# Kernel optimization log

Measured on AMD Instinct MI355X. Metric: run time of the kernel, lower is better.

Reference implementation:

```python
import jax, jax.numpy as jnp
import numpy as np

IN_F = 1024
OUT_F = 1024
N_ORDER = 13  # grid_size=10 + spline_order=3
RMS_EPS = 1e-6


def setup_inputs() -> dict:
    key = jax.random.key(0)
    k_x, k_b, k_p = jax.random.split(key, 3)
    x = jax.random.normal(k_x, (4, 2048, IN_F), dtype=jnp.float32)
    # flax param init: normal(stddev=scale_base/sqrt(in_features)) etc.
    base_weight = jax.random.normal(k_b, (IN_F, OUT_F), dtype=jnp.float32) * (1.0 / np.sqrt(IN_F))
    poly_weight = jax.random.normal(k_p, (N_ORDER, IN_F, OUT_F), dtype=jnp.float32) * (0.1 / np.sqrt(IN_F * N_ORDER))
    rms_scale = jnp.ones((OUT_F,), dtype=jnp.float32)  # nn.RMSNorm default scale init
    return {"x": x, "base_weight": base_weight, "poly_weight": poly_weight, "rms_scale": rms_scale}


def reference(x, base_weight, poly_weight, rms_scale):
    orig_dtype = x.dtype
    prefix = x.shape[:-1]
    x_2d = x.reshape(-1, IN_F)  # [B, in]

    # Base path: SiLU(x) @ W_base in bf16
    x_c = x_2d.astype(jnp.bfloat16)
    out = jax.nn.silu(x_c) @ base_weight.astype(jnp.bfloat16)  # [B, out] bf16

    # Chebyshev recursion on tanh-normalized fp32 input
    x_safe = jnp.tanh(x_2d.astype(jnp.float32))
    pw = poly_weight.astype(jnp.bfloat16)
    T_prev = jnp.ones_like(x_safe)
    T_curr = x_safe
    out = out + T_prev.astype(jnp.bfloat16) @ pw[0]
    out = out + T_curr.astype(jnp.bfloat16) @ pw[1]
    for k in range(2, N_ORDER):  # fixed small unroll (13 orders)
        T_next = 2.0 * x_safe * T_curr - T_prev
        out = out + T_next.astype(jnp.bfloat16) @ pw[k]
        T_prev = T_curr
        T_curr = T_next

    # RMSNorm (flax default: eps=1e-6, learned scale)
    o32 = out.astype(jnp.float32)
    ms = jnp.mean(o32 * o32, axis=-1, keepdims=True)
    o32 = o32 * jax.lax.rsqrt(ms + RMS_EPS) * rms_scale
    return o32.astype(orig_dtype).reshape(prefix + (OUT_F,))
```

## Files before the change

kernel.cpp:

```cpp
#include <hip/hip_runtime.h>
#include <cstdint>

#define IN_F  1024
#define OUT_F 1024
#define NORD  13
#define BROWS 8192

typedef __bf16 bf16x8 __attribute__((ext_vector_type(8)));
typedef float  f32x4  __attribute__((ext_vector_type(4)));
typedef unsigned short u16x8 __attribute__((ext_vector_type(8)));
typedef unsigned short u16x4 __attribute__((ext_vector_type(4)));

__device__ __forceinline__ unsigned short f2bf(float f) {
  unsigned int u = __float_as_uint(f);
  unsigned int r = u + 0x7FFFu + ((u >> 16) & 1u);
  return (unsigned short)(r >> 16);
}
__device__ __forceinline__ float bf2f(unsigned short h) {
  return __uint_as_float(((unsigned int)h) << 16);
}
__device__ __forceinline__ float bfround(float f) { return bf2f(f2bf(f)); }

__device__ __forceinline__ float fast_tanh(float x) {
  float e = __expf(2.0f * x);
  return 1.0f - 2.0f / (e + 1.0f);
}

__device__ __forceinline__ void gload_lds16(const void* g, void* l) {
  __builtin_amdgcn_global_load_lds(
      (__attribute__((address_space(1))) unsigned int*)(uintptr_t)g,
      (__attribute__((address_space(3))) unsigned int*)(unsigned int)(uintptr_t)l,
      16, 0, 0);
}

__global__ __launch_bounds__(256)
void act_kernel(const float* __restrict__ x, unsigned short* __restrict__ A,
                int b0, int nb, int Kp) {
  int t   = threadIdx.x;
  int row = blockIdx.x * 2 + (t >> 7);
  int f0  = (t & 127) * 8;
  const float* xr = x + (size_t)row * IN_F + f0;
  float xv[8];
  *(float4*)&xv[0] = *(const float4*)&xr[0];
  *(float4*)&xv[4] = *(const float4*)&xr[4];
  unsigned short* Ar = A + (size_t)row * Kp;
  int omax = b0 + nb - 1;
  if (b0 == 0) {
    u16x8 sv;
#pragma unroll
    for (int i = 0; i < 8; i++) {
      float xc = bfround(xv[i]);
      float sg = bfround(1.0f / (1.0f + __expf(-xc)));
      sv[i] = f2bf(xc * sg);
    }
    *(u16x8*)&Ar[f0] = sv;
  }
  float xs[8], tp[8], tc[8];
#pragma unroll
  for (int i = 0; i < 8; i++) { xs[i] = fast_tanh(xv[i]); tp[i] = 1.0f; tc[i] = xs[i]; }
  for (int o = 1; o <= omax; o++) {
    if (o >= b0) {
      int bb = o - b0;
      u16x8 sv;
#pragma unroll
      for (int i = 0; i < 8; i++) sv[i] = f2bf(tc[i]);
      *(u16x8*)&Ar[(size_t)bb * 1024 + f0] = sv;
    }
    {
#pragma clang fp contract(off)
#pragma unroll
      for (int i = 0; i < 8; i++) {
        float tm = 2.0f * xs[i] * tc[i];
        float tn = tm - tp[i];
        tp[i] = tc[i]; tc[i] = tn;
      }
    }
  }
}

__global__ __launch_bounds__(256)
void wprep_kernel(const float* __restrict__ baseW, const float* __restrict__ poly,
                  unsigned short* __restrict__ Wt, int b0, int Kp) {
  __shared__ float tile[64][65];
  int bb = blockIdx.z;
  int g  = b0 + bb;
  const float* src = (g == 0) ? baseW : (poly + (size_t)g * (IN_F * OUT_F));
  int n0 = blockIdx.x * 64, f0 = blockIdx.y * 64;
  int tx = threadIdx.x, ty = threadIdx.y;
#pragma unroll
  for (int i = 0; i < 16; i++)
    tile[ty + i * 4][tx] = src[(size_t)(f0 + ty + i * 4) * OUT_F + n0 + tx];
  __syncthreads();
#pragma unroll
  for (int i = 0; i < 16; i++)
    Wt[(size_t)(n0 + ty + i * 4) * Kp + (size_t)bb * 1024 + f0 + tx] = f2bf(tile[tx][ty + i * 4]);
}

__global__ __launch_bounds__(256)
void bias1_kernel(const float* __restrict__ pw0, float* __restrict__ partial) {
  int t  = threadIdx.x;
  int n  = blockIdx.x * 256 + t;
  int fc = blockIdx.y;
  float s = 0.f;
  for (int f = fc * 128; f < fc * 128 + 128; f++)
    s += bf2f(f2bf(pw0[(size_t)f * OUT_F + n]));
  partial[(size_t)fc * OUT_F + n] = s;
}
__global__ __launch_bounds__(256)
void bias2_kernel(const float* __restrict__ partial, float* __restrict__ bias) {
  int n = blockIdx.x * 256 + threadIdx.x;
  float s = 0.f;
#pragma unroll
  for (int fc = 0; fc < 8; fc++) s += partial[(size_t)fc * OUT_F + n];
  bias[n] = s;
}

__global__ __launch_bounds__(256, 2)
void gemm_kernel(const unsigned short* __restrict__ A, const unsigned short* __restrict__ Wt,
                 unsigned short* __restrict__ outAcc, const float* __restrict__ bias,
                 int Kp, int isFirst) {
  __shared__ unsigned short sA[2][128 * 64];
  __shared__ unsigned short sB[2][128 * 64];
  int t    = threadIdx.x;
  int m0   = blockIdx.x * 128;
  int n0   = blockIdx.y * 128;
  int wave = t >> 6, lane = t & 63;
  int lr   = lane & 15, quad = lane >> 4;
  int wm   = (wave & 1) * 64, wn = (wave >> 1) * 64;

  int rs = t >> 3;
  int jg = (t & 7) ^ (rs & 7);
  const unsigned short* aSrc = A  + (size_t)(m0 + rs) * Kp + jg * 8;
  const unsigned short* bSrc = Wt + (size_t)(n0 + rs) * Kp + jg * 8;
  char* sAc = (char*)sA;
  char* sBc = (char*)sB;
  int ldsOff = t * 16;

  int aOff[4][2], bOff[4][2];
#pragma unroll
  for (int mi = 0; mi < 4; mi++) {
    int row = wm + mi * 16 + lr;
#pragma unroll
    for (int ks = 0; ks < 2; ks++) {
      int j = ks * 4 + quad;
      aOff[mi][ks] = row * 128 + ((j ^ (row & 7)) * 16);
    }
  }
#pragma unroll
  for (int ni = 0; ni < 4; ni++) {
    int row = wn + ni * 16 + lr;
#pragma unroll
    for (int ks = 0; ks < 2; ks++) {
      int j = ks * 4 + quad;
      bOff[ni][ks] = row * 128 + ((j ^ (row & 7)) * 16);
    }
  }

  f32x4 s[4][4];
  float bsr[4];
  if (isFirst) {
#pragma unroll
    for (int ni = 0; ni < 4; ni++) bsr[ni] = bfround(bias[n0 + wn + ni * 16 + lr]);
  } else {
#pragma unroll
    for (int ni = 0; ni < 4; ni++) {
      int gn = n0 + wn + ni * 16 + lr;
#pragma unroll
      for (int mi = 0; mi < 4; mi++) {
        int gmBase = m0 + wm + mi * 16 + quad * 4;
#pragma unroll
        for (int r = 0; r < 4; r++)
          s[mi][ni][r] = bf2f(outAcc[(size_t)(gmBase + r) * OUT_F + gn]);
      }
    }
  }

  int nKt  = Kp >> 6;
  int nBlk = Kp >> 10;

  auto stage = [&](int gkt, int buf) {
    const unsigned short* aP = aSrc + gkt * 64;
    const unsigned short* bP = bSrc + gkt * 64;
    char* dA = sAc + buf * 16384 + ldsOff;
    char* dB = sBc + buf * 16384 + ldsOff;
#pragma unroll
    for (int rd = 0; rd < 4; rd++)
      gload_lds16(aP + (size_t)rd * 32 * Kp, dA + rd * 4096);
#pragma unroll
    for (int rd = 0; rd < 4; rd++)
      gload_lds16(bP + (size_t)rd * 32 * Kp, dB + rd * 4096);
  };

  stage(0, 0);
  stage(1, 1);

  int gkt   = 0;
  int nKtm1 = nKt - 1;
  for (int blk = 0; blk < nBlk; blk++) {
    f32x4 acc[4][4];
#pragma unroll
    for (int mi = 0; mi < 4; mi++)
#pragma unroll
      for (int ni = 0; ni < 4; ni++)
        acc[mi][ni] = (f32x4){0.f, 0.f, 0.f, 0.f};

    for (int kt = 0; kt < 16; kt++, gkt++) {
      if (gkt != nKtm1) {
        asm volatile("s_waitcnt vmcnt(8)" ::: "memory");
      } else {
        asm volatile("s_waitcnt vmcnt(0)" ::: "memory");
      }
      __builtin_amdgcn_s_barrier();
      __builtin_amdgcn_sched_barrier(0);

      int buf = gkt & 1;
      char* bA = sAc + buf * 16384;
      char* bB = sBc + buf * 16384;
      bf16x8 af[2][4], bfr[2][4];
#pragma unroll
      for (int ks = 0; ks < 2; ks++) {
#pragma unroll
        for (int mi = 0; mi < 4; mi++) af[ks][mi] = *(const bf16x8*)(bA + aOff[mi][ks]);
#pragma unroll
        for (int ni = 0; ni < 4; ni++) bfr[ks][ni] = *(const bf16x8*)(bB + bOff[ni][ks]);
      }
      asm volatile("s_waitcnt lgkmcnt(0)" ::: "memory");
      __builtin_amdgcn_s_barrier();
      __builtin_amdgcn_sched_barrier(0);

      int nxt = gkt + 2;
      if (nxt < nKt) stage(nxt, buf);

#pragma unroll
      for (int ks = 0; ks < 2; ks++)
#pragma unroll
        for (int mi = 0; mi < 4; mi++)
#pragma unroll
          for (int ni = 0; ni < 4; ni++)
            acc[mi][ni] = __builtin_amdgcn_mfma_f32_16x16x32_bf16(af[ks][mi], bfr[ks][ni], acc[mi][ni], 0, 0, 0);
    }

    bool firstBlk = (isFirst && blk == 0);
    if (firstBlk) {
#pragma unroll
      for (int mi = 0; mi < 4; mi++)
#pragma unroll
        for (int ni = 0; ni < 4; ni++)
#pragma unroll
          for (int r = 0; r < 4; r++) {
            float p = bfround(acc[mi][ni][r]);
            s[mi][ni][r] = bfround(p + bsr[ni]);
          }
    } else {
#pragma unroll
      for (int mi = 0; mi < 4; mi++)
#pragma unroll
        for (int ni = 0; ni < 4; ni++)
#pragma unroll
          for (int r = 0; r < 4; r++)
            s[mi][ni][r] = bfround(s[mi][ni][r] + bfround(acc[mi][ni][r]));
    }
  }

#pragma unroll
  for (int ni = 0; ni < 4; ni++) {
    int gn = n0 + wn + ni * 16 + lr;
#pragma unroll
    for (int mi = 0; mi < 4; mi++) {
      int gmBase = m0 + wm + mi * 16 + quad * 4;
#pragma unroll
      for (int r = 0; r < 4; r++)
        outAcc[(size_t)(gmBase + r) * OUT_F + gn] = f2bf(s[mi][ni][r]);
    }
  }
}

__global__ __launch_bounds__(256)
void rms_kernel(const unsigned short* __restrict__ outAcc, const float* __restrict__ scale,
                float* __restrict__ out) {
  int row = blockIdx.x;
  int t   = threadIdx.x;
  const unsigned short* src = outAcc + (size_t)row * OUT_F;
  u16x4 hv = *(const u16x4*)&src[t * 4];
  float v[4];
#pragma unroll
  for (int i = 0; i < 4; i++) v[i] = bf2f(hv[i]);
  float s = v[0]*v[0] + v[1]*v[1] + v[2]*v[2] + v[3]*v[3];
#pragma unroll
  for (int off = 32; off > 0; off >>= 1) s += __shfl_down(s, off, 64);
  __shared__ float red[4];
  if ((t & 63) == 0) red[t >> 6] = s;
  __syncthreads();
  float tot = red[0] + red[1] + red[2] + red[3];
  float sc = 1.0f / sqrtf(tot * (1.0f / OUT_F) + 1e-6f);
  float4 so = *(const float4*)&scale[t * 4];
  float4 o;
  o.x = v[0] * sc * so.x; o.y = v[1] * sc * so.y;
  o.z = v[2] * sc * so.z; o.w = v[3] * sc * so.w;
  *(float4*)&out[(size_t)row * OUT_F + t * 4] = o;
}

extern "C" void kernel_launch(void* const* d_in, const int* in_sizes, int n_in,
                              void* d_out, int out_size, void* d_ws, size_t ws_size,
                              hipStream_t stream) {
  const float* x     = (const float*)d_in[0];
  const float* baseW = (const float*)d_in[1];
  const float* poly  = (const float*)d_in[2];
  const float* scale = (const float*)d_in[3];
  float* out = (float*)d_out;

  char* ws = (char*)d_ws;
  unsigned short* outAcc = (unsigned short*)ws;
  float* bias    = (float*)(ws + 16777216);
  float* partial = (float*)(ws + 16777216 + 4096);
  size_t fixed   = 16777216 + 4096 + 32768;

  int CHB = 1;
  for (int c = NORD; c >= 1; c--) {
    size_t need = fixed + (size_t)c * 1024 * OUT_F * 2
                + (size_t)BROWS * c * 1024 * 2;
    if (need <= ws_size) { CHB = c; break; }
  }
  unsigned short* Wt = (unsigned short*)(ws + fixed);
  unsigned short* Ap = (unsigned short*)(ws + fixed + (size_t)CHB * 1024 * OUT_F * 2);

  bias1_kernel<<<dim3(4, 8), 256, 0, stream>>>(poly, partial);
  bias2_kernel<<<4, 256, 0, stream>>>(partial, bias);

  for (int b0 = 0; b0 < NORD; b0 += CHB) {
    int nb = (CHB < NORD - b0) ? CHB : (NORD - b0);
    int Kp = nb * 1024;
    act_kernel<<<BROWS / 2, 256, 0, stream>>>(x, Ap, b0, nb, Kp);
    wprep_kernel<<<dim3(16, 16, nb), dim3(64, 4), 0, stream>>>(baseW, poly, Wt, b0, Kp);
    gemm_kernel<<<dim3(BROWS / 128, 8), 256, 0, stream>>>(Ap, Wt, outAcc, bias, Kp, (b0 == 0) ? 1 : 0);
  }
  rms_kernel<<<BROWS, 256, 0, stream>>>(outAcc, scale, out);
}
```

Measured before the change: 431.9 us.

## Use triple-buffered K=32 LDS tiles with a single barrier per step

The GEMM main loop moves from double-buffered 64-wide K tiles to triple-buffered 32-wide K tiles, with a new XOR swizzle. The next stage is issued before the current tile is read, so one barrier per iteration is removed and prefetch overlaps the LDS reads and MFMAs. In exchange each step runs half as many MFMAs per barrier and the loop has twice as many iterations. The Chebyshev prep also precomputes 2*tanh(x) once instead of multiplying by 2 in every iteration.

```diff
diff --git a/kernel.cpp b/kernel.cpp
--- a/kernel.cpp
+++ b/kernel.cpp
@@ -55,9 +55,12 @@
     }
     *(u16x8*)&Ar[f0] = sv;
   }
-  float xs[8], tp[8], tc[8];
-#pragma unroll
-  for (int i = 0; i < 8; i++) { xs[i] = fast_tanh(xv[i]); tp[i] = 1.0f; tc[i] = xs[i]; }
+  float xs2[8], tp[8], tc[8];
+#pragma unroll
+  for (int i = 0; i < 8; i++) {
+    float xs = fast_tanh(xv[i]);
+    tp[i] = 1.0f; tc[i] = xs; xs2[i] = xs + xs;
+  }
   for (int o = 1; o <= omax; o++) {
     if (o >= b0) {
       int bb = o - b0;
@@ -70,7 +73,7 @@
 #pragma clang fp contract(off)
 #pragma unroll
       for (int i = 0; i < 8; i++) {
-        float tm = 2.0f * xs[i] * tc[i];
+        float tm = xs2[i] * tc[i];
         float tn = tm - tp[i];
         tp[i] = tc[i]; tc[i] = tn;
       }
@@ -119,8 +122,8 @@
 void gemm_kernel(const unsigned short* __restrict__ A, const unsigned short* __restrict__ Wt,
                  unsigned short* __restrict__ outAcc, const float* __restrict__ bias,
                  int Kp, int isFirst) {
-  __shared__ unsigned short sA[2][128 * 64];
-  __shared__ unsigned short sB[2][128 * 64];
+  __shared__ unsigned short sA[3][128 * 32];
+  __shared__ unsigned short sB[3][128 * 32];
   int t    = threadIdx.x;
   int m0   = blockIdx.x * 128;
   int n0   = blockIdx.y * 128;
@@ -128,32 +131,25 @@
   int lr   = lane & 15, quad = lane >> 4;
   int wm   = (wave & 1) * 64, wn = (wave >> 1) * 64;
 
-  int rs = t >> 3;
-  int jg = (t & 7) ^ (rs & 7);
+  int rs = t >> 2;
+  int jg = (t & 3) ^ ((t >> 3) & 3);
   const unsigned short* aSrc = A  + (size_t)(m0 + rs) * Kp + jg * 8;
   const unsigned short* bSrc = Wt + (size_t)(n0 + rs) * Kp + jg * 8;
   char* sAc = (char*)sA;
   char* sBc = (char*)sB;
   int ldsOff = t * 16;
 
-  int aOff[4][2], bOff[4][2];
+  int g4 = (lr >> 1) & 3;
+  int aOff[4], bOff[4];
 #pragma unroll
   for (int mi = 0; mi < 4; mi++) {
     int row = wm + mi * 16 + lr;
-#pragma unroll
-    for (int ks = 0; ks < 2; ks++) {
-      int j = ks * 4 + quad;
-      aOff[mi][ks] = row * 128 + ((j ^ (row & 7)) * 16);
-    }
+    aOff[mi] = row * 64 + ((quad ^ g4) * 16);
   }
 #pragma unroll
   for (int ni = 0; ni < 4; ni++) {
     int row = wn + ni * 16 + lr;
-#pragma unroll
-    for (int ks = 0; ks < 2; ks++) {
-      int j = ks * 4 + quad;
-      bOff[ni][ks] = row * 128 + ((j ^ (row & 7)) * 16);
-    }
+    bOff[ni] = row * 64 + ((quad ^ g4) * 16);
   }
 
   f32x4 s[4][4];
@@ -175,26 +171,25 @@
     }
   }
 
-  int nKt  = Kp >> 6;
+  int nKt  = Kp >> 5;
   int nBlk = Kp >> 10;
 
   auto stage = [&](int gkt, int buf) {
-    const unsigned short* aP = aSrc + gkt * 64;
-    const unsigned short* bP = bSrc + gkt * 64;
-    char* dA = sAc + buf * 16384 + ldsOff;
-    char* dB = sBc + buf * 16384 + ldsOff;
-#pragma unroll
-    for (int rd = 0; rd < 4; rd++)
-      gload_lds16(aP + (size_t)rd * 32 * Kp, dA + rd * 4096);
-#pragma unroll
-    for (int rd = 0; rd < 4; rd++)
-      gload_lds16(bP + (size_t)rd * 32 * Kp, dB + rd * 4096);
+    const unsigned short* aP = aSrc + gkt * 32;
+    const unsigned short* bP = bSrc + gkt * 32;
+    char* dA = sAc + buf * 8192 + ldsOff;
+    char* dB = sBc + buf * 8192 + ldsOff;
+    gload_lds16(aP,                     dA);
+    gload_lds16(aP + (size_t)64 * Kp,   dA + 4096);
+    gload_lds16(bP,                     dB);
+    gload_lds16(bP + (size_t)64 * Kp,   dB + 4096);
   };
 
   stage(0, 0);
   stage(1, 1);
 
   int gkt   = 0;
+  int bufC  = 0;
   int nKtm1 = nKt - 1;
   for (int blk = 0; blk < nBlk; blk++) {
     f32x4 acc[4][4];
@@ -204,40 +199,35 @@
       for (int ni = 0; ni < 4; ni++)
         acc[mi][ni] = (f32x4){0.f, 0.f, 0.f, 0.f};
 
-    for (int kt = 0; kt < 16; kt++, gkt++) {
+    for (int kt = 0; kt < 32; kt++, gkt++) {
       if (gkt != nKtm1) {
-        asm volatile("s_waitcnt vmcnt(8)" ::: "memory");
+        asm volatile("s_waitcnt vmcnt(4)" ::: "memory");
       } else {
         asm volatile("s_waitcnt vmcnt(0)" ::: "memory");
       }
       __builtin_amdgcn_s_barrier();
       __builtin_amdgcn_sched_barrier(0);
 
-      int buf = gkt & 1;
-      char* bA = sAc + buf * 16384;
-      char* bB = sBc + buf * 16384;
-      bf16x8 af[2][4], bfr[2][4];
-#pragma unroll
-      for (int ks = 0; ks < 2; ks++) {
-#pragma unroll
-        for (int mi = 0; mi < 4; mi++) af[ks][mi] = *(const bf16x8*)(bA + aOff[mi][ks]);
-#pragma unroll
-        for (int ni = 0; ni < 4; ni++) bfr[ks][ni] = *(const bf16x8*)(bB + bOff[ni][ks]);
+      int nxt = gkt + 2;
+      if (nxt < nKt) {
+        int bufN = bufC + 2; if (bufN >= 3) bufN -= 3;
+        stage(nxt, bufN);
       }
-      asm volatile("s_waitcnt lgkmcnt(0)" ::: "memory");
-      __builtin_amdgcn_s_barrier();
-      __builtin_amdgcn_sched_barrier(0);
-
-      int nxt = gkt + 2;
-      if (nxt < nKt) stage(nxt, buf);
-
-#pragma unroll
-      for (int ks = 0; ks < 2; ks++)
-#pragma unroll
-        for (int mi = 0; mi < 4; mi++)
-#pragma unroll
-          for (int ni = 0; ni < 4; ni++)
-            acc[mi][ni] = __builtin_amdgcn_mfma_f32_16x16x32_bf16(af[ks][mi], bfr[ks][ni], acc[mi][ni], 0, 0, 0);
+
+      char* bA = sAc + bufC * 8192;
+      char* bB = sBc + bufC * 8192;
+      bf16x8 af[4], bfv[4];
+#pragma unroll
+      for (int mi = 0; mi < 4; mi++) af[mi] = *(const bf16x8*)(bA + aOff[mi]);
+#pragma unroll
+      for (int ni = 0; ni < 4; ni++) bfv[ni] = *(const bf16x8*)(bB + bOff[ni]);
+#pragma unroll
+      for (int mi = 0; mi < 4; mi++)
+#pragma unroll
+        for (int ni = 0; ni < 4; ni++)
+          acc[mi][ni] = __builtin_amdgcn_mfma_f32_16x16x32_bf16(af[mi], bfv[ni], acc[mi][ni], 0, 0, 0);
+
+      bufC++; if (bufC == 3) bufC = 0;
     }
 
     bool firstBlk = (isFirst && blk == 0);
```

Measured after the change: 460.2 us. +6.6%, slower.

## Enlarge GEMM tile to 256x128 with 512 threads and triple-buffered LDS

Applied to the files above, without the earlier changes.

The GEMM block doubles its M tile to 256 rows and runs 8 waves. LDS staging moves from double to triple buffering, which lets the next-next tile load be issued before the current tile is read and drops one barrier per k-step. LDS fragment loads are now interleaved per k-substep with the MFMAs. The act kernel also precomputes 2*tanh(x) once for the Chebyshev recurrence. This is meant to cut barrier stalls and global traffic per FLOP, at the cost of larger LDS use and only one block per CU.

```diff
diff --git a/kernel.cpp b/kernel.cpp
--- a/kernel.cpp
+++ b/kernel.cpp
@@ -55,9 +55,12 @@
     }
     *(u16x8*)&Ar[f0] = sv;
   }
-  float xs[8], tp[8], tc[8];
-#pragma unroll
-  for (int i = 0; i < 8; i++) { xs[i] = fast_tanh(xv[i]); tp[i] = 1.0f; tc[i] = xs[i]; }
+  float xs2[8], tp[8], tc[8];
+#pragma unroll
+  for (int i = 0; i < 8; i++) {
+    float xs = fast_tanh(xv[i]);
+    tp[i] = 1.0f; tc[i] = xs; xs2[i] = xs + xs;
+  }
   for (int o = 1; o <= omax; o++) {
     if (o >= b0) {
       int bb = o - b0;
@@ -70,7 +73,7 @@
 #pragma clang fp contract(off)
 #pragma unroll
       for (int i = 0; i < 8; i++) {
-        float tm = 2.0f * xs[i] * tc[i];
+        float tm = xs2[i] * tc[i];
         float tn = tm - tp[i];
         tp[i] = tc[i]; tc[i] = tn;
       }
@@ -115,18 +118,18 @@
   bias[n] = s;
 }
 
-__global__ __launch_bounds__(256, 2)
+__global__ __launch_bounds__(512, 1)
 void gemm_kernel(const unsigned short* __restrict__ A, const unsigned short* __restrict__ Wt,
                  unsigned short* __restrict__ outAcc, const float* __restrict__ bias,
                  int Kp, int isFirst) {
-  __shared__ unsigned short sA[2][128 * 64];
-  __shared__ unsigned short sB[2][128 * 64];
+  __shared__ unsigned short sA[3][256 * 64];
+  __shared__ unsigned short sB[3][128 * 64];
   int t    = threadIdx.x;
-  int m0   = blockIdx.x * 128;
+  int m0   = blockIdx.x * 256;
   int n0   = blockIdx.y * 128;
   int wave = t >> 6, lane = t & 63;
   int lr   = lane & 15, quad = lane >> 4;
-  int wm   = (wave & 1) * 64, wn = (wave >> 1) * 64;
+  int wm   = (wave >> 1) * 64, wn = (wave & 1) * 64;
 
   int rs = t >> 3;
   int jg = (t & 7) ^ (rs & 7);
@@ -178,23 +181,24 @@
   int nKt  = Kp >> 6;
   int nBlk = Kp >> 10;
 
-  auto stage = [&](int gkt, int buf) {
-    const unsigned short* aP = aSrc + gkt * 64;
-    const unsigned short* bP = bSrc + gkt * 64;
-    char* dA = sAc + buf * 16384 + ldsOff;
+  auto stage = [&](int g, int buf) {
+    const unsigned short* aP = aSrc + (size_t)g * 64;
+    const unsigned short* bP = bSrc + (size_t)g * 64;
+    char* dA = sAc + buf * 32768 + ldsOff;
     char* dB = sBc + buf * 16384 + ldsOff;
 #pragma unroll
     for (int rd = 0; rd < 4; rd++)
-      gload_lds16(aP + (size_t)rd * 32 * Kp, dA + rd * 4096);
-#pragma unroll
-    for (int rd = 0; rd < 4; rd++)
-      gload_lds16(bP + (size_t)rd * 32 * Kp, dB + rd * 4096);
+      gload_lds16(aP + (size_t)rd * 64 * Kp, dA + rd * 8192);
+#pragma unroll
+    for (int rd = 0; rd < 2; rd++)
+      gload_lds16(bP + (size_t)rd * 64 * Kp, dB + rd * 8192);
   };
 
   stage(0, 0);
   stage(1, 1);
 
   int gkt   = 0;
+  int bufC  = 0;
   int nKtm1 = nKt - 1;
   for (int blk = 0; blk < nBlk; blk++) {
     f32x4 acc[4][4];
@@ -206,38 +210,36 @@
 
     for (int kt = 0; kt < 16; kt++, gkt++) {
       if (gkt != nKtm1) {
-        asm volatile("s_waitcnt vmcnt(8)" ::: "memory");
+        asm volatile("s_waitcnt vmcnt(6)" ::: "memory");
       } else {
         asm volatile("s_waitcnt vmcnt(0)" ::: "memory");
       }
       __builtin_amdgcn_s_barrier();
       __builtin_amdgcn_sched_barrier(0);
 
-      int buf = gkt & 1;
-      char* bA = sAc + buf * 16384;
-      char* bB = sBc + buf * 16384;
-      bf16x8 af[2][4], bfr[2][4];
+      int nxt2 = gkt + 2;
+      if (nxt2 < nKt) {
+        int bufN = bufC + 2; if (bufN >= 3) bufN -= 3;
+        stage(nxt2, bufN);
+      }
+
+      const char* bA = sAc + bufC * 32768;
+      const char* bB = sBc + bufC * 16384;
 #pragma unroll
       for (int ks = 0; ks < 2; ks++) {
-#pragma unroll
-        for (int mi = 0; mi < 4; mi++) af[ks][mi] = *(const bf16x8*)(bA + aOff[mi][ks]);
-#pragma unroll
-        for (int ni = 0; ni < 4; ni++) bfr[ks][ni] = *(const bf16x8*)(bB + bOff[ni][ks]);
-      }
-      asm volatile("s_waitcnt lgkmcnt(0)" ::: "memory");
-      __builtin_amdgcn_s_barrier();
-      __builtin_amdgcn_sched_barrier(0);
-
-      int nxt = gkt + 2;
-      if (nxt < nKt) stage(nxt, buf);
-
-#pragma unroll
-      for (int ks = 0; ks < 2; ks++)
+        bf16x8 af[4], bfr[4];
+#pragma unroll
+        for (int mi = 0; mi < 4; mi++) af[mi] = *(const bf16x8*)(bA + aOff[mi][ks]);
+#pragma unroll
+        for (int ni = 0; ni < 4; ni++) bfr[ni] = *(const bf16x8*)(bB + bOff[ni][ks]);
 #pragma unroll
         for (int mi = 0; mi < 4; mi++)
 #pragma unroll
           for (int ni = 0; ni < 4; ni++)
-            acc[mi][ni] = __builtin_amdgcn_mfma_f32_16x16x32_bf16(af[ks][mi], bfr[ks][ni], acc[mi][ni], 0, 0, 0);
+            acc[mi][ni] = __builtin_amdgcn_mfma_f32_16x16x32_bf16(af[mi], bfr[ni], acc[mi][ni], 0, 0, 0);
+      }
+
+      bufC++; if (bufC == 3) bufC = 0;
     }
 
     bool firstBlk = (isFirst && blk == 0);
@@ -332,7 +334,7 @@
     int Kp = nb * 1024;
     act_kernel<<<BROWS / 2, 256, 0, stream>>>(x, Ap, b0, nb, Kp);
     wprep_kernel<<<dim3(16, 16, nb), dim3(64, 4), 0, stream>>>(baseW, poly, Wt, b0, Kp);
-    gemm_kernel<<<dim3(BROWS / 128, 8), 256, 0, stream>>>(Ap, Wt, outAcc, bias, Kp, (b0 == 0) ? 1 : 0);
+    gemm_kernel<<<dim3(BROWS / 256, 8), 512, 0, stream>>>(Ap, Wt, outAcc, bias, Kp, (b0 == 0) ? 1 : 0);
   }
   rms_kernel<<<BROWS, 256, 0, stream>>>(outAcc, scale, out);
 }
```

Result: faster. 406.5 us (-5.9%).
